# Optimization experiments

Hardware: AMD Instinct MI355X
Metric: run time of the kernel (lower is better)

The kernel has to match this reference:

```python
import jax, jax.numpy as jnp
import numpy as np

B, C, IN_DIM, OUT_DIM, H = 8, 2048, 128, 128, 4
D = OUT_DIM // H  # d_k = 32


def setup_inputs() -> dict:
    key = jax.random.key(0)
    ks = jax.random.split(key, 7)
    s = 1.0 / np.sqrt(IN_DIM)
    x = jax.random.normal(ks[0], (B, C, IN_DIM), dtype=jnp.float32)
    adj = jax.random.uniform(ks[1], (B, C, C), dtype=jnp.float32)
    Wq = jax.random.uniform(ks[2], (IN_DIM, H * D), jnp.float32, -s, s)
    Wk = jax.random.uniform(ks[3], (IN_DIM, H * D), jnp.float32, -s, s)
    Wv = jax.random.uniform(ks[4], (IN_DIM, H * D), jnp.float32, -s, s)
    so = 1.0 / np.sqrt(H * D)
    Wo = jax.random.uniform(ks[5], (H * D, OUT_DIM), jnp.float32, -so, so)
    bo = jax.random.uniform(ks[6], (OUT_DIM,), jnp.float32, -so, so)
    return {"x": x, "adj": adj, "Wq": Wq, "Wk": Wk, "Wv": Wv, "Wo": Wo, "bo": bo}


def reference(x, adj, Wq, Wk, Wv, Wo, bo):
    # Project to per-head Q/K/V: (B, H, C, D)
    def proj(W):
        return (x @ W).reshape(B, C, H, D).transpose(0, 2, 1, 3)
    Q, K, V = proj(Wq), proj(Wk), proj(Wv)
    # Scaled dot-product scores, adjacency-gated, LeakyReLU(0.2), softmax
    scores = jnp.einsum('bhqd,bhkd->bhqk', Q, K) / jnp.sqrt(jnp.float32(D))
    scores = scores * adj[:, None, :, :]
    scores = jnp.where(scores > 0, scores, 0.2 * scores)  # LeakyReLU(0.2)
    attn = jax.nn.softmax(scores, axis=-1)  # dropout is identity at eval
    out = jnp.einsum('bhqk,bhkd->bhqd', attn, V)
    out = out.transpose(0, 2, 1, 3).reshape(B, C, H * D)  # concat heads
    return out @ Wo + bo
```

## Files before the change

### kernel.cpp

```cpp
#include <hip/hip_runtime.h>
#include <hip/hip_bf16.h>

constexpr int B_  = 8;
constexpr int C_  = 2048;
constexpr int IND = 128;
constexpr int H_  = 4;
constexpr int D_  = 32;
constexpr int M_  = B_ * C_;
constexpr float QSCALE = 0.17677669529663687f;
constexpr float L2E    = 1.4426950408889634f;
constexpr float QL2    = QSCALE * L2E;

constexpr int KSPLIT = 4;
constexpr int KPG = C_ / KSPLIT;

typedef __attribute__((ext_vector_type(8))) short short8;
typedef __attribute__((ext_vector_type(4))) short s4t;
typedef __attribute__((ext_vector_type(4))) float f4t;
typedef __attribute__((ext_vector_type(4))) unsigned short us4;

#if __has_builtin(__builtin_amdgcn_mfma_f32_16x16x16bf16_1k)
#define MFMA16(a, b, c) __builtin_amdgcn_mfma_f32_16x16x16bf16_1k(a, b, c, 0, 0, 0)
#else
#define MFMA16(a, b, c) (c)
#endif
#define MFMA32(a, b, c) __builtin_amdgcn_mfma_f32_16x16x32_bf16(a, b, c, 0, 0, 0)

__device__ __forceinline__ unsigned short f2bf(float f) {
    union { float f; unsigned u; } v; v.f = f;
    unsigned u = v.u + 0x7fffu + ((v.u >> 16) & 1u);
    return (unsigned short)(u >> 16);
}

__device__ __forceinline__ s4t pack4_bf16(float p0, float p1, float p2, float p3) {
#if __has_builtin(__builtin_amdgcn_cvt_pk_bf16_f32)
    auto a = __builtin_amdgcn_cvt_pk_bf16_f32(p0, p1);
    auto b = __builtin_amdgcn_cvt_pk_bf16_f32(p2, p3);
    unsigned u[2];
    __builtin_memcpy(&u[0], &a, 4);
    __builtin_memcpy(&u[1], &b, 4);
    s4t pp;
    __builtin_memcpy(&pp, u, 8);
    return pp;
#else
    s4t pp;
    pp[0] = (short)f2bf(p0); pp[1] = (short)f2bf(p1);
    pp[2] = (short)f2bf(p2); pp[3] = (short)f2bf(p3);
    return pp;
#endif
}

__device__ __forceinline__ short8 cvt8(float4 a, float4 b) {
    s4t x = pack4_bf16(a.x, a.y, a.z, a.w);
    s4t y = pack4_bf16(b.x, b.y, b.z, b.w);
    short8 r;
    r[0] = x[0]; r[1] = x[1]; r[2] = x[2]; r[3] = x[3];
    r[4] = y[0]; r[5] = y[1]; r[6] = y[2]; r[7] = y[3];
    return r;
}

__global__ __launch_bounds__(256) void prep_w_kernel(
    const float* __restrict__ Wq, const float* __restrict__ Wk,
    const float* __restrict__ Wv, const float* __restrict__ Wo,
    unsigned short* __restrict__ Wtb)
{
    __shared__ unsigned short lds[16][130];
    const int t  = threadIdx.x;
    const int n0 = blockIdx.x * 16;

    const float* src; int nb; float sc = 1.0f;
    if      (n0 < 128) { src = Wq; nb = n0;       sc = QL2; }
    else if (n0 < 256) { src = Wk; nb = n0 - 128; }
    else if (n0 < 384) { src = Wv; nb = n0 - 256; }
    else               { src = Wo; nb = n0 - 384; }

    const int nn = t & 15, kk = t >> 4;
#pragma unroll
    for (int kb = 0; kb < 8; ++kb) {
        const int k = kb * 16 + kk;
        lds[nn][k] = f2bf(src[k * IND + nb + nn] * sc);
    }
    __syncthreads();
    const int k = t & 127, rr = t >> 7;
#pragma unroll
    for (int it = 0; it < 8; ++it) {
        const int r = it * 2 + rr;
        Wtb[(size_t)(n0 + r) * IND + k] = lds[r][k];
    }
}

__global__ __launch_bounds__(192) void qkv_proj_kernel(
    const float* __restrict__ x, const unsigned short* __restrict__ Wtb,
    unsigned short* __restrict__ Qb, unsigned short* __restrict__ Kb,
    unsigned short* __restrict__ Vt)
{
    const int t = threadIdx.x;
    const int w = t >> 6;
    const int l = t & 63;
    const int lo = l & 15, hi = l >> 4;
    const int tok0 = blockIdx.x * 16;
    const int b  = tok0 >> 11;
    const int cb = tok0 & 2047;
    const int tile0 = blockIdx.y * 4;

    short8 xb[4];
    const float* xrow = x + (size_t)(tok0 + lo) * IND;
#pragma unroll
    for (int kc = 0; kc < 4; ++kc) {
        const float4 a = *(const float4*)(xrow + kc * 32 + hi * 8);
        const float4 c = *(const float4*)(xrow + kc * 32 + hi * 8 + 4);
        xb[kc] = cvt8(a, c);
    }

    const unsigned short* wbase = Wtb + (size_t)(w * 128) * IND;
#pragma unroll
    for (int tile = 0; tile < 4; ++tile) {
        const int n0 = (tile0 + tile) * 16;
        short8 wf[4];
#pragma unroll
        for (int kc = 0; kc < 4; ++kc)
            wf[kc] = *(const short8*)(wbase + (size_t)(n0 + lo) * IND +
                                      kc * 32 + hi * 8);
        f4t acc = 0.f;
        if (w < 2) {
#pragma unroll
            for (int kc = 0; kc < 4; ++kc) acc = MFMA32(wf[kc], xb[kc], acc);
            us4 v;
#pragma unroll
            for (int r = 0; r < 4; ++r) v[r] = f2bf(acc[r]);
            unsigned short* O = (w == 0) ? Qb : Kb;
            *(us4*)(O + (size_t)(tok0 + lo) * IND + n0 + hi * 4) = v;
        } else {
#pragma unroll
            for (int kc = 0; kc < 4; ++kc) acc = MFMA32(xb[kc], wf[kc], acc);
            us4 v;
#pragma unroll
            for (int r = 0; r < 4; ++r) v[r] = f2bf(acc[r]);
            *(us4*)(Vt + ((size_t)(b * IND) + n0 + lo) * C_ + cb + hi * 4) = v;
        }
    }
}

__global__ __launch_bounds__(256, 3) void attn_kernel(
    const unsigned short* __restrict__ Qb, const unsigned short* __restrict__ Kb,
    const unsigned short* __restrict__ Vt, const float* __restrict__ adj,
    float* __restrict__ Opart, float* __restrict__ lpart)
{
    __shared__ __align__(16) char Ksm[2][8192];
    __shared__ __align__(16) char Vsm[2][8192];
    __shared__ __align__(16) char Asm[2][8192];

    const int t  = threadIdx.x;
    const int s  = t >> 6;
    const int l  = t & 63;
    const int lo = l & 15, hi = l >> 4;
    const int b  = blockIdx.y;
    const int kz = blockIdx.z;
    const int q0 = blockIdx.x * 64;
    const int qs = q0 + s * 16 + lo;
    const int kzoff = kz * KPG;
    const int NCH = KPG / 32;

    const int x7 = (lo & 7) << 4;
    const int x3 = (lo & 3) << 4;

    const int keyA = s * 8 + (l >> 4);
    const int keyB = keyA + 4;
    const char* srcK_A = (const char*)Kb + ((size_t)(b * C_ + kzoff) + keyA) * 256
                         + (((l & 15) * 16) ^ ((keyA & 7) << 4));
    const char* srcK_B = (const char*)Kb + ((size_t)(b * C_ + kzoff) + keyB) * 256
                         + (((l & 15) * 16) ^ ((keyB & 7) << 4));
    const int dA = s * 32 + (l >> 2);
    const int dB = dA + 16;
    const char* srcV_A = (const char*)Vt + (size_t)(b * IND + dA) * (C_ * 2)
                         + (size_t)kzoff * 2
                         + (((l & 3) * 16) ^ ((dA & 3) << 4));
    const char* srcV_B = (const char*)Vt + (size_t)(b * IND + dB) * (C_ * 2)
                         + (size_t)kzoff * 2
                         + (((l & 3) * 16) ^ ((dB & 3) << 4));
    const int qA = s * 16 + (l >> 3);
    const int qB = qA + 8;
    const char* srcA_A = (const char*)adj + ((size_t)(b * C_ + q0 + qA) * C_ + kzoff) * 4
                         + (((l & 7) * 16) ^ ((qA & 7) << 4));
    const char* srcA_B = (const char*)adj + ((size_t)(b * C_ + q0 + qB) * C_ + kzoff) * 4
                         + (((l & 7) * 16) ^ ((qB & 7) << 4));

#if __has_builtin(__builtin_amdgcn_global_load_lds)
#define GLL(gp, lp) __builtin_amdgcn_global_load_lds( \
    (const __attribute__((address_space(1))) unsigned int*)(gp), \
    (__attribute__((address_space(3))) unsigned int*)(lp), 16, 0, 0)
#else
#define GLL(gp, lp) (void)(gp)
#endif

    auto stage = [&](int c, int buf) {
        GLL(srcK_A + (size_t)c * 8192, Ksm[buf] + (2 * s)     * 1024);
        GLL(srcK_B + (size_t)c * 8192, Ksm[buf] + (2 * s + 1) * 1024);
        GLL(srcV_A + (size_t)c * 64,   Vsm[buf] + (2 * s)     * 1024);
        GLL(srcV_B + (size_t)c * 64,   Vsm[buf] + (2 * s + 1) * 1024);
        GLL(srcA_A + (size_t)c * 128,  Asm[buf] + (2 * s)     * 1024);
        GLL(srcA_B + (size_t)c * 128,  Asm[buf] + (2 * s + 1) * 1024);
    };

    short8 qf[4];
#pragma unroll
    for (int h = 0; h < 4; ++h)
        qf[h] = *(const short8*)(Qb + ((size_t)(b * C_) + qs) * IND + h * 32 + hi * 8);
    __builtin_amdgcn_sched_barrier(0);
    stage(0, 0);
    __builtin_amdgcn_sched_barrier(0);
    stage(1, 1);
    __builtin_amdgcn_sched_barrier(0);

    f4t acc[4][2];
#pragma unroll
    for (int h = 0; h < 4; ++h) { acc[h][0] = 0.f; acc[h][1] = 0.f; }
    float ls[4] = {0.f, 0.f, 0.f, 0.f};

    auto computeC = [&](int buf, int st) {
        const char* Kl = Ksm[buf];
        const char* Vl = Vsm[buf];
        const char* Al = Asm[buf];
        short8 kf[4];
#pragma unroll
        for (int h = 0; h < 4; ++h)
            kf[h] = *(const short8*)(Kl + (st * 16 + lo) * 256 +
                                     ((h * 64 + hi * 16) ^ x7));
        s4t vf[8];
#pragma unroll
        for (int h = 0; h < 4; ++h) {
            vf[h * 2]     = *(const s4t*)(Vl + (h * 32 + lo) * 64 +
                                          ((st * 32 + hi * 8) ^ x3));
            vf[h * 2 + 1] = *(const s4t*)(Vl + (h * 32 + 16 + lo) * 64 +
                                          ((st * 32 + hi * 8) ^ x3));
        }
        const f4t av = *(const f4t*)(Al + (s * 16 + lo) * 128 +
                                     ((st * 64 + hi * 16) ^ x7));
#pragma unroll
        for (int h = 0; h < 4; ++h) {
            f4t st4 = MFMA32(kf[h], qf[h], (f4t)0.f);
            float p[4];
#pragma unroll
            for (int r = 0; r < 4; ++r) {
                const float a = st4[r] * av[r];
                const float m = fmaxf(a, 0.2f * a);
                p[r] = exp2f(m);
                ls[h] += p[r];
            }
            const s4t pp = pack4_bf16(p[0], p[1], p[2], p[3]);
            acc[h][0] = MFMA16(pp, vf[h * 2], acc[h][0]);
            acc[h][1] = MFMA16(pp, vf[h * 2 + 1], acc[h][1]);
        }
    };

    for (int c = 0; c < NCH; ++c) {
        if (c + 1 < NCH) { asm volatile("s_waitcnt vmcnt(6)" ::: "memory"); }
        else             { asm volatile("s_waitcnt vmcnt(0)" ::: "memory"); }
        __builtin_amdgcn_sched_barrier(0);
        __builtin_amdgcn_s_barrier();
        __builtin_amdgcn_sched_barrier(0);

        computeC(c & 1, 0);
        computeC(c & 1, 1);

        asm volatile("s_waitcnt lgkmcnt(0)" ::: "memory");
        __builtin_amdgcn_sched_barrier(0);
        __builtin_amdgcn_s_barrier();
        __builtin_amdgcn_sched_barrier(0);
        if (c + 2 < NCH) stage(c + 2, c & 1);
    }

#pragma unroll
    for (int h = 0; h < 4; ++h) {
        ls[h] += __shfl_xor(ls[h], 16, 64);
        ls[h] += __shfl_xor(ls[h], 32, 64);
    }

    const size_t BHC   = (size_t)B_ * H_ * C_;
    const size_t obase = (size_t)kz * BHC;

    const float lw = (hi == 0) ? ls[0] : (hi == 1) ? ls[1] : (hi == 2) ? ls[2] : ls[3];
    lpart[obase + (size_t)(b * H_ + hi) * C_ + qs] = lw;

#pragma unroll
    for (int h = 0; h < 4; ++h) {
        const size_t rb = obase + (size_t)(b * H_ + h) * C_ + q0 + s * 16 + hi * 4;
#pragma unroll
        for (int dh = 0; dh < 2; ++dh)
#pragma unroll
            for (int r = 0; r < 4; ++r)
                Opart[(rb + r) * D_ + dh * 16 + lo] = acc[h][dh][r];
    }
#undef GLL
}

__global__ __launch_bounds__(256) void combine_kernel(
    const float* __restrict__ Opart, const float* __restrict__ lpart,
    unsigned short* __restrict__ AOb)
{
    const int cid = blockIdx.x * 256 + threadIdx.x;
    const int j   = cid & 7;
    const int idx = cid >> 3;
    const int q  = idx & (C_ - 1);
    const int bh = idx >> 11;
    const int h  = bh & (H_ - 1);
    const int b  = bh >> 2;
    const size_t BHC = (size_t)B_ * H_ * C_;

    float4 acc = {0.f, 0.f, 0.f, 0.f};
    float lsum = 0.f;
#pragma unroll
    for (int kz = 0; kz < KSPLIT; ++kz) {
        const size_t base = (size_t)kz * BHC + idx;
        lsum += lpart[base];
        const float4 v = *(const float4*)(Opart + base * D_ + j * 4);
        acc.x += v.x; acc.y += v.y; acc.z += v.z; acc.w += v.w;
    }
    const float inv = 1.f / lsum;
    us4 o;
    o[0] = f2bf(acc.x * inv); o[1] = f2bf(acc.y * inv);
    o[2] = f2bf(acc.z * inv); o[3] = f2bf(acc.w * inv);
    *(us4*)(AOb + ((size_t)(b * C_) + q) * IND + h * D_ + j * 4) = o;
}

__global__ __launch_bounds__(256) void out_proj_kernel(
    const unsigned short* __restrict__ AOb, const unsigned short* __restrict__ Wtb,
    const float* __restrict__ bo, float* __restrict__ out)
{
    const int t  = threadIdx.x;
    const int w  = t >> 6;
    const int l  = t & 63;
    const int lo = l & 15, hi = l >> 4;
    const int tok0 = blockIdx.x * 16;

    short8 af[4];
    const unsigned short* arow = AOb + (size_t)(tok0 + lo) * IND;
#pragma unroll
    for (int kc = 0; kc < 4; ++kc)
        af[kc] = *(const short8*)(arow + kc * 32 + hi * 8);

    const unsigned short* wbase = Wtb + (size_t)384 * IND;
#pragma unroll
    for (int tt = 0; tt < 2; ++tt) {
        const int n0 = w * 32 + tt * 16;
        short8 wf[4];
#pragma unroll
        for (int kc = 0; kc < 4; ++kc)
            wf[kc] = *(const short8*)(wbase + (size_t)(n0 + lo) * IND +
                                      kc * 32 + hi * 8);
        f4t acc = 0.f;
#pragma unroll
        for (int kc = 0; kc < 4; ++kc) acc = MFMA32(wf[kc], af[kc], acc);
        const f4t bv = *(const f4t*)(bo + n0 + hi * 4);
        float4 o;
        o.x = acc[0] + bv[0]; o.y = acc[1] + bv[1];
        o.z = acc[2] + bv[2]; o.w = acc[3] + bv[3];
        *(float4*)(out + (size_t)(tok0 + lo) * IND + n0 + hi * 4) = o;
    }
}

extern "C" void kernel_launch(void* const* d_in, const int* in_sizes, int n_in,
                              void* d_out, int out_size, void* d_ws, size_t ws_size,
                              hipStream_t stream) {
    const float* x   = (const float*)d_in[0];
    const float* adj = (const float*)d_in[1];
    const float* Wq  = (const float*)d_in[2];
    const float* Wk  = (const float*)d_in[3];
    const float* Wv  = (const float*)d_in[4];
    const float* Wo  = (const float*)d_in[5];
    const float* bo  = (const float*)d_in[6];
    float* out = (float*)d_out;

    unsigned short* Wtb = (unsigned short*)d_ws;
    unsigned short* Qb  = Wtb + (size_t)512 * IND;
    unsigned short* Kb  = Qb + (size_t)M_ * IND;
    unsigned short* Vt  = Kb + (size_t)M_ * IND;
    unsigned short* AOb = Vt + (size_t)M_ * IND;
    float* Opart = (float*)(AOb + (size_t)M_ * IND);
    float* lpart = Opart + (size_t)KSPLIT * B_ * H_ * C_ * D_;

    hipLaunchKernelGGL(prep_w_kernel, dim3(32), dim3(256), 0, stream,
                       Wq, Wk, Wv, Wo, Wtb);
    hipLaunchKernelGGL(qkv_proj_kernel, dim3(M_ / 16, 2), dim3(192), 0, stream,
                       x, Wtb, Qb, Kb, Vt);
    hipLaunchKernelGGL(attn_kernel, dim3(C_ / 64, B_, KSPLIT), dim3(256), 0, stream,
                       Qb, Kb, Vt, adj, Opart, lpart);
    hipLaunchKernelGGL(combine_kernel, dim3(B_ * H_ * C_ * 8 / 256), dim3(256), 0, stream,
                       Opart, lpart, AOb);
    hipLaunchKernelGGL(out_proj_kernel, dim3(M_ / 16), dim3(256), 0, stream,
                       AOb, Wtb, bo, out);
}
```

Measured before the change: 287.0 us.

## Halve attention chunk to 16 keys to shrink LDS and raise occupancy

Each pipeline stage in the attention kernel now covers 16 keys instead of 32. This halves the K, V and adjacency LDS buffers (48KB to 24KB) and lets launch bounds ask for 4 blocks per SM instead of 3. The XOR swizzle on the V and adjacency LDS layouts is dropped because the rows are now narrower, and each stage issues 3 async loads instead of 6, with the vmcnt wait adjusted to match. The trade-off is twice as many barrier pairs per key range, smaller transfers per stage, and possible LDS bank conflicts on the unswizzled V and adj reads.

```diff
diff --git a/kernel.cpp b/kernel.cpp
--- a/kernel.cpp
+++ b/kernel.cpp
@@ -141,14 +141,14 @@
     }
 }
 
-__global__ __launch_bounds__(256, 3) void attn_kernel(
+__global__ __launch_bounds__(256, 4) void attn_kernel(
     const unsigned short* __restrict__ Qb, const unsigned short* __restrict__ Kb,
     const unsigned short* __restrict__ Vt, const float* __restrict__ adj,
     float* __restrict__ Opart, float* __restrict__ lpart)
 {
-    __shared__ __align__(16) char Ksm[2][8192];
-    __shared__ __align__(16) char Vsm[2][8192];
-    __shared__ __align__(16) char Asm[2][8192];
+    __shared__ __align__(16) char Ksm[2][4096];
+    __shared__ __align__(16) char Vsm[2][4096];
+    __shared__ __align__(16) char Asm[2][4096];
 
     const int t  = threadIdx.x;
     const int s  = t >> 6;
@@ -159,31 +159,18 @@
     const int q0 = blockIdx.x * 64;
     const int qs = q0 + s * 16 + lo;
     const int kzoff = kz * KPG;
-    const int NCH = KPG / 32;
-
-    const int x7 = (lo & 7) << 4;
-    const int x3 = (lo & 3) << 4;
-
-    const int keyA = s * 8 + (l >> 4);
-    const int keyB = keyA + 4;
-    const char* srcK_A = (const char*)Kb + ((size_t)(b * C_ + kzoff) + keyA) * 256
-                         + (((l & 15) * 16) ^ ((keyA & 7) << 4));
-    const char* srcK_B = (const char*)Kb + ((size_t)(b * C_ + kzoff) + keyB) * 256
-                         + (((l & 15) * 16) ^ ((keyB & 7) << 4));
-    const int dA = s * 32 + (l >> 2);
-    const int dB = dA + 16;
-    const char* srcV_A = (const char*)Vt + (size_t)(b * IND + dA) * (C_ * 2)
-                         + (size_t)kzoff * 2
-                         + (((l & 3) * 16) ^ ((dA & 3) << 4));
-    const char* srcV_B = (const char*)Vt + (size_t)(b * IND + dB) * (C_ * 2)
-                         + (size_t)kzoff * 2
-                         + (((l & 3) * 16) ^ ((dB & 3) << 4));
-    const int qA = s * 16 + (l >> 3);
-    const int qB = qA + 8;
-    const char* srcA_A = (const char*)adj + ((size_t)(b * C_ + q0 + qA) * C_ + kzoff) * 4
-                         + (((l & 7) * 16) ^ ((qA & 7) << 4));
-    const char* srcA_B = (const char*)adj + ((size_t)(b * C_ + q0 + qB) * C_ + kzoff) * 4
-                         + (((l & 7) * 16) ^ ((qB & 7) << 4));
+    const int NCH = KPG / 16;
+
+    const int keyS = s * 4 + (l >> 4);
+    const char* srcK = (const char*)Kb + ((size_t)(b * C_ + kzoff) + keyS) * 256
+                       + (((l & 15) * 16) ^ ((keyS & 7) << 4));
+    const int dS = s * 32 + (l >> 1);
+    const char* srcV = (const char*)Vt + (size_t)(b * IND + dS) * (C_ * 2)
+                       + (size_t)kzoff * 2 + (l & 1) * 16;
+    const int qS = s * 16 + (l >> 2);
+    const char* srcA = (const char*)adj
+                       + ((size_t)(b * C_ + q0 + qS) * C_ + kzoff) * 4
+                       + (l & 3) * 16;
 
 #if __has_builtin(__builtin_amdgcn_global_load_lds)
 #define GLL(gp, lp) __builtin_amdgcn_global_load_lds( \
@@ -194,12 +181,9 @@
 #endif
 
     auto stage = [&](int c, int buf) {
-        GLL(srcK_A + (size_t)c * 8192, Ksm[buf] + (2 * s)     * 1024);
-        GLL(srcK_B + (size_t)c * 8192, Ksm[buf] + (2 * s + 1) * 1024);
-        GLL(srcV_A + (size_t)c * 64,   Vsm[buf] + (2 * s)     * 1024);
-        GLL(srcV_B + (size_t)c * 64,   Vsm[buf] + (2 * s + 1) * 1024);
-        GLL(srcA_A + (size_t)c * 128,  Asm[buf] + (2 * s)     * 1024);
-        GLL(srcA_B + (size_t)c * 128,  Asm[buf] + (2 * s + 1) * 1024);
+        GLL(srcK + (size_t)c * 4096, Ksm[buf] + s * 1024);
+        GLL(srcV + (size_t)c * 32,   Vsm[buf] + s * 1024);
+        GLL(srcA + (size_t)c * 64,   Asm[buf] + s * 1024);
     };
 
     short8 qf[4];
@@ -217,25 +201,23 @@
     for (int h = 0; h < 4; ++h) { acc[h][0] = 0.f; acc[h][1] = 0.f; }
     float ls[4] = {0.f, 0.f, 0.f, 0.f};
 
-    auto computeC = [&](int buf, int st) {
+    const int x7 = (lo & 7) << 4;
+
+    auto computeC = [&](int buf) {
         const char* Kl = Ksm[buf];
         const char* Vl = Vsm[buf];
         const char* Al = Asm[buf];
         short8 kf[4];
 #pragma unroll
         for (int h = 0; h < 4; ++h)
-            kf[h] = *(const short8*)(Kl + (st * 16 + lo) * 256 +
-                                     ((h * 64 + hi * 16) ^ x7));
+            kf[h] = *(const short8*)(Kl + lo * 256 + ((h * 64 + hi * 16) ^ x7));
         s4t vf[8];
 #pragma unroll
         for (int h = 0; h < 4; ++h) {
-            vf[h * 2]     = *(const s4t*)(Vl + (h * 32 + lo) * 64 +
-                                          ((st * 32 + hi * 8) ^ x3));
-            vf[h * 2 + 1] = *(const s4t*)(Vl + (h * 32 + 16 + lo) * 64 +
-                                          ((st * 32 + hi * 8) ^ x3));
+            vf[h * 2]     = *(const s4t*)(Vl + (h * 32 + lo) * 32 + hi * 8);
+            vf[h * 2 + 1] = *(const s4t*)(Vl + (h * 32 + 16 + lo) * 32 + hi * 8);
         }
-        const f4t av = *(const f4t*)(Al + (s * 16 + lo) * 128 +
-                                     ((st * 64 + hi * 16) ^ x7));
+        const f4t av = *(const f4t*)(Al + (s * 16 + lo) * 64 + hi * 16);
 #pragma unroll
         for (int h = 0; h < 4; ++h) {
             f4t st4 = MFMA32(kf[h], qf[h], (f4t)0.f);
@@ -254,14 +236,13 @@
     };
 
     for (int c = 0; c < NCH; ++c) {
-        if (c + 1 < NCH) { asm volatile("s_waitcnt vmcnt(6)" ::: "memory"); }
+        if (c + 1 < NCH) { asm volatile("s_waitcnt vmcnt(3)" ::: "memory"); }
         else             { asm volatile("s_waitcnt vmcnt(0)" ::: "memory"); }
         __builtin_amdgcn_sched_barrier(0);
         __builtin_amdgcn_s_barrier();
         __builtin_amdgcn_sched_barrier(0);
 
-        computeC(c & 1, 0);
-        computeC(c & 1, 1);
+        computeC(c & 1);
 
         asm volatile("s_waitcnt lgkmcnt(0)" ::: "memory");
         __builtin_amdgcn_sched_barrier(0);
```

New measurement: 286.5 us. Within noise of the previous version (-0.2%).

## Load V fragments directly from global memory instead of staging in LDS

Applied to the files above, without the earlier changes.

Drops the LDS double buffer for the transposed V tile and has each lane read its V fragments straight from global memory inside the score loop. The prefetch wait count is adjusted to match the smaller number of staged loads, and launch bounds rise from 3 to 4 blocks per CU to use the freed LDS. The adjacency swizzle is rewritten in an equivalent form. The V reads are now issued behind the staged K and adjacency prefetches in the same in-order vector-memory counter, so waiting on them may also force a wait on the prefetched next-chunk loads and weaken the double buffering. The four waves also each re-read the same V data from cache.

```diff
diff --git a/kernel.cpp b/kernel.cpp
--- a/kernel.cpp
+++ b/kernel.cpp
@@ -141,13 +141,12 @@
     }
 }
 
-__global__ __launch_bounds__(256, 3) void attn_kernel(
+__global__ __launch_bounds__(256, 4) void attn_kernel(
     const unsigned short* __restrict__ Qb, const unsigned short* __restrict__ Kb,
     const unsigned short* __restrict__ Vt, const float* __restrict__ adj,
     float* __restrict__ Opart, float* __restrict__ lpart)
 {
     __shared__ __align__(16) char Ksm[2][8192];
-    __shared__ __align__(16) char Vsm[2][8192];
     __shared__ __align__(16) char Asm[2][8192];
 
     const int t  = threadIdx.x;
@@ -161,29 +160,18 @@
     const int kzoff = kz * KPG;
     const int NCH = KPG / 32;
 
-    const int x7 = (lo & 7) << 4;
-    const int x3 = (lo & 3) << 4;
-
-    const int keyA = s * 8 + (l >> 4);
-    const int keyB = keyA + 4;
-    const char* srcK_A = (const char*)Kb + ((size_t)(b * C_ + kzoff) + keyA) * 256
-                         + (((l & 15) * 16) ^ ((keyA & 7) << 4));
-    const char* srcK_B = (const char*)Kb + ((size_t)(b * C_ + kzoff) + keyB) * 256
-                         + (((l & 15) * 16) ^ ((keyB & 7) << 4));
-    const int dA = s * 32 + (l >> 2);
-    const int dB = dA + 16;
-    const char* srcV_A = (const char*)Vt + (size_t)(b * IND + dA) * (C_ * 2)
-                         + (size_t)kzoff * 2
-                         + (((l & 3) * 16) ^ ((dA & 3) << 4));
-    const char* srcV_B = (const char*)Vt + (size_t)(b * IND + dB) * (C_ * 2)
-                         + (size_t)kzoff * 2
-                         + (((l & 3) * 16) ^ ((dB & 3) << 4));
+    const int kA = s * 8 + (l >> 4);
+    const int kB = kA + 4;
+    const char* srcK_A = (const char*)Kb + ((size_t)(b * C_ + kzoff) + kA) * 256
+                         + (((l & 15) * 16) ^ ((kA & 7) << 4));
+    const char* srcK_B = (const char*)Kb + ((size_t)(b * C_ + kzoff) + kB) * 256
+                         + (((l & 15) * 16) ^ ((kB & 7) << 4));
     const int qA = s * 16 + (l >> 3);
     const int qB = qA + 8;
     const char* srcA_A = (const char*)adj + ((size_t)(b * C_ + q0 + qA) * C_ + kzoff) * 4
-                         + (((l & 7) * 16) ^ ((qA & 7) << 4));
+                         + (((l & 7) * 16) ^ ((l >> 3) << 4));
     const char* srcA_B = (const char*)adj + ((size_t)(b * C_ + q0 + qB) * C_ + kzoff) * 4
-                         + (((l & 7) * 16) ^ ((qB & 7) << 4));
+                         + (((l & 7) * 16) ^ ((l >> 3) << 4));
 
 #if __has_builtin(__builtin_amdgcn_global_load_lds)
 #define GLL(gp, lp) __builtin_amdgcn_global_load_lds( \
@@ -196,8 +184,6 @@
     auto stage = [&](int c, int buf) {
         GLL(srcK_A + (size_t)c * 8192, Ksm[buf] + (2 * s)     * 1024);
         GLL(srcK_B + (size_t)c * 8192, Ksm[buf] + (2 * s + 1) * 1024);
-        GLL(srcV_A + (size_t)c * 64,   Vsm[buf] + (2 * s)     * 1024);
-        GLL(srcV_B + (size_t)c * 64,   Vsm[buf] + (2 * s + 1) * 1024);
         GLL(srcA_A + (size_t)c * 128,  Asm[buf] + (2 * s)     * 1024);
         GLL(srcA_B + (size_t)c * 128,  Asm[buf] + (2 * s + 1) * 1024);
     };
@@ -217,27 +203,24 @@
     for (int h = 0; h < 4; ++h) { acc[h][0] = 0.f; acc[h][1] = 0.f; }
     float ls[4] = {0.f, 0.f, 0.f, 0.f};
 
-    auto computeC = [&](int buf, int st) {
+    const unsigned short* Vrow = Vt + ((size_t)(b * IND) + lo) * C_ + hi * 4;
+    const int x7 = (lo & 7) << 4;
+
+    auto computeS = [&](int buf, int c, int st) {
         const char* Kl = Ksm[buf];
-        const char* Vl = Vsm[buf];
         const char* Al = Asm[buf];
+        const int k0 = kzoff + c * 32 + st * 16;
         short8 kf[4];
 #pragma unroll
         for (int h = 0; h < 4; ++h)
             kf[h] = *(const short8*)(Kl + (st * 16 + lo) * 256 +
                                      ((h * 64 + hi * 16) ^ x7));
-        s4t vf[8];
-#pragma unroll
-        for (int h = 0; h < 4; ++h) {
-            vf[h * 2]     = *(const s4t*)(Vl + (h * 32 + lo) * 64 +
-                                          ((st * 32 + hi * 8) ^ x3));
-            vf[h * 2 + 1] = *(const s4t*)(Vl + (h * 32 + 16 + lo) * 64 +
-                                          ((st * 32 + hi * 8) ^ x3));
-        }
         const f4t av = *(const f4t*)(Al + (s * 16 + lo) * 128 +
                                      ((st * 64 + hi * 16) ^ x7));
 #pragma unroll
         for (int h = 0; h < 4; ++h) {
+            const s4t vf0 = *(const s4t*)(Vrow + (size_t)(h * 32) * C_ + k0);
+            const s4t vf1 = *(const s4t*)(Vrow + (size_t)(h * 32 + 16) * C_ + k0);
             f4t st4 = MFMA32(kf[h], qf[h], (f4t)0.f);
             float p[4];
 #pragma unroll
@@ -248,20 +231,20 @@
                 ls[h] += p[r];
             }
             const s4t pp = pack4_bf16(p[0], p[1], p[2], p[3]);
-            acc[h][0] = MFMA16(pp, vf[h * 2], acc[h][0]);
-            acc[h][1] = MFMA16(pp, vf[h * 2 + 1], acc[h][1]);
+            acc[h][0] = MFMA16(pp, vf0, acc[h][0]);
+            acc[h][1] = MFMA16(pp, vf1, acc[h][1]);
         }
     };
 
     for (int c = 0; c < NCH; ++c) {
-        if (c + 1 < NCH) { asm volatile("s_waitcnt vmcnt(6)" ::: "memory"); }
+        if (c + 1 < NCH) { asm volatile("s_waitcnt vmcnt(4)" ::: "memory"); }
         else             { asm volatile("s_waitcnt vmcnt(0)" ::: "memory"); }
         __builtin_amdgcn_sched_barrier(0);
         __builtin_amdgcn_s_barrier();
         __builtin_amdgcn_sched_barrier(0);
 
-        computeC(c & 1, 0);
-        computeC(c & 1, 1);
+        computeS(c & 1, c, 0);
+        computeS(c & 1, c, 1);
 
         asm volatile("s_waitcnt lgkmcnt(0)" ::: "memory");
         __builtin_amdgcn_sched_barrier(0);
```

Measured after the change: 336.6 us. +17.2%, slower.
